# Kernel optimization log

Hardware: AMD Instinct MI355X
Metric: run time of the kernel (lower is better)

## Reference

```python
import jax, jax.numpy as jnp
import numpy as np

# Fixed architecture constants from Cifar10Model / RetNetConfig
NL = 8            # num_layers
H = 4             # num_heads
D = 64            # hidden_size
QK = 64           # qk_dim
V = 128           # v_dim
QH, VH = QK // H, V // H   # 16, 32 per-head dims
P, IMG, C = 8, 32, 3       # patch size, image size, channels
NP = (IMG // P) ** 2       # 16 patches
T = NP + 1                 # +1 cls token -> 17 tokens
FFN = 12                   # ffn_proj_size


def layer_norm(x, s, b, eps=1e-5):
    mu = x.mean(-1, keepdims=True)
    var = x.var(-1, keepdims=True)
    return (x - mu) * jax.lax.rsqrt(var + eps) * s + b


def rotate_every_two(x):
    x1, x2 = x[..., ::2], x[..., 1::2]
    return jnp.stack([-x2, x1], axis=-1).reshape(x.shape)


def rel_pos(t):
    # xPos-style rotation angles over the per-head qk dim
    angle = 1.0 / (10000 ** jnp.linspace(0.0, 1.0, QH // 2))
    angle = jnp.repeat(angle, 2)                      # (QH,)
    idx = jnp.arange(t, dtype=jnp.float32)[:, None]
    sin, cos = jnp.sin(idx * angle), jnp.cos(idx * angle)   # (t, QH)
    # per-head retention decay gamma (use_default_gamma=False path)
    gamma = 1.0 - jnp.exp(jnp.linspace(np.log(1 / 32), np.log(1 / 512), H))  # (H,)
    n = jnp.arange(t)
    expo = n[:, None] - n[None, :]                    # n - m
    causal = expo >= 0
    dmask = jnp.where(causal, gamma[:, None, None] ** jnp.where(causal, expo, 0), 0.0)  # (H,t,t)
    dmask = dmask / jnp.sqrt(dmask.sum(-1, keepdims=True))   # row-normalized decay
    return sin, cos, dmask


def retention(x, Wq, Wk, Wv, Wg, Wo, sin, cos, dmask):
    b, t, _ = x.shape
    q = (x @ Wq).reshape(b, t, H, QH).transpose(0, 2, 1, 3)   # (b,h,t,qh)
    k = (x @ Wk).reshape(b, t, H, QH).transpose(0, 2, 1, 3)
    v = (x @ Wv).reshape(b, t, H, VH).transpose(0, 2, 1, 3)   # (b,h,t,vh)
    g = x @ Wg                                                # (b,t,V) gate
    q = q * cos + rotate_every_two(q) * sin
    k = (k * cos + rotate_every_two(k) * sin) * (QH ** -0.5)
    scores = jnp.einsum('bhnd,bhmd->bhnm', q, k) * dmask      # decay-masked QK^T
    denom = jnp.clip(jnp.abs(jax.lax.stop_gradient(scores).sum(-1, keepdims=True)), 1.0, None)
    scores = scores / denom                                   # retention row normalization
    o = jnp.einsum('bhnm,bhmd->bhnd', scores, v)              # (b,h,t,vh)
    # per-head group norm (no affine) instead of softmax normalization
    mu = o.mean(-1, keepdims=True)
    var = o.var(-1, keepdims=True)
    o = (o - mu) * jax.lax.rsqrt(var + 1e-5)
    o = o.transpose(0, 2, 1, 3).reshape(b, t, V)
    return (jax.nn.silu(g) * o) @ Wo


def setup_inputs() -> dict:
    key = jax.random.key(0)
    ks = iter(jax.random.split(key, 32))
    s = 0.02
    B = 8192
    inp = {
        'x': jax.random.normal(next(ks), (B, C, IMG, IMG), jnp.float32),
        'patch_w': jax.random.normal(next(ks), (C * P * P, D), jnp.float32) * s,
        'patch_b': jnp.zeros((D,), jnp.float32),
        'cls': jax.random.normal(next(ks), (1, 1, D), jnp.float32) * s,
        'pos': jax.random.normal(next(ks), (T, D), jnp.float32) * s,
        'Wq': jax.random.normal(next(ks), (NL, D, QK), jnp.float32) * s,
        'Wk': jax.random.normal(next(ks), (NL, D, QK), jnp.float32) * s,
        'Wv': jax.random.normal(next(ks), (NL, D, V), jnp.float32) * s,
        'Wg': jax.random.normal(next(ks), (NL, D, V), jnp.float32) * s,
        'Wo': jax.random.normal(next(ks), (NL, V, D), jnp.float32) * s,
        'ln1_s': jnp.ones((NL, D), jnp.float32),
        'ln1_b': jnp.zeros((NL, D), jnp.float32),
        'w1': jax.random.normal(next(ks), (NL, D, FFN), jnp.float32) * s,
        'b1': jnp.zeros((NL, FFN), jnp.float32),
        'w2': jax.random.normal(next(ks), (NL, FFN, D), jnp.float32) * s,
        'b2': jnp.zeros((NL, D), jnp.float32),
        'ln2_s': jnp.ones((NL, D), jnp.float32),
        'ln2_b': jnp.zeros((NL, D), jnp.float32),
        'lnf_s': jnp.ones((D,), jnp.float32),
        'lnf_b': jnp.zeros((D,), jnp.float32),
        'neck_w': jax.random.normal(next(ks), (D, 16), jnp.float32) * s,
        'neck_b': jnp.zeros((16,), jnp.float32),
        'head_w': jax.random.normal(next(ks), (16, 10), jnp.float32) * s,
        'head_b': jnp.zeros((10,), jnp.float32),
    }
    return inp


def reference(x, patch_w, patch_b, cls, pos, Wq, Wk, Wv, Wg, Wo, ln1_s, ln1_b,
              w1, b1, w2, b2, ln2_s, ln2_b, lnf_s, lnf_b, neck_w, neck_b, head_w, head_b):
    b = x.shape[0]
    # patch embedding: stride==kernel conv expressed as reshape + matmul
    xp = x.reshape(b, C, IMG // P, P, IMG // P, P).transpose(0, 2, 4, 1, 3, 5)
    xp = xp.reshape(b, NP, C * P * P)
    tok = xp @ patch_w + patch_b                          # (b,16,64)
    tok = jnp.concatenate([jnp.broadcast_to(cls, (b, 1, D)), tok], axis=1) + pos  # (b,17,64)
    sin, cos, dmask = rel_pos(T)
    h = tok
    for i in range(NL):  # pre-LN RetNet blocks
        h = h + retention(layer_norm(h, ln1_s[i], ln1_b[i]),
                          Wq[i], Wk[i], Wv[i], Wg[i], Wo[i], sin, cos, dmask)
        f = layer_norm(h, ln2_s[i], ln2_b[i])
        h = h + jax.nn.gelu(f @ w1[i] + b1[i]) @ w2[i] + b2[i]
    h = layer_norm(h, lnf_s, lnf_b)
    ys = h[:, -1, :]                                      # last token
    return (ys @ neck_w + neck_b) @ head_w + head_b       # (b,10) logits
```

## Files before the change

kernel.cpp:

```cpp
#include <hip/hip_runtime.h>
#include <hip/hip_bf16.h>

#define NLAY 8
#define MFMA __builtin_amdgcn_mfma_f32_16x16x32_bf16
#define MFMA32 __builtin_amdgcn_mfma_f32_32x32x16_bf16

typedef __attribute__((ext_vector_type(8))) short bf16x8;
typedef __attribute__((ext_vector_type(4))) float f32x4;
typedef __attribute__((ext_vector_type(16))) float f32x16;
typedef __attribute__((ext_vector_type(4))) int i32x4;

template <bool BF16>
__device__ __forceinline__ float ld(const void* p, int i) {
  if (BF16) {
    unsigned short u = ((const unsigned short*)p)[i];
    return __uint_as_float(((unsigned)u) << 16);
  }
  return ((const float*)p)[i];
}

template <bool BF16>
__device__ __forceinline__ float2 ld2(const void* p, int i) {
  float2 r;
  if (BF16) {
    unsigned u = ((const unsigned*)p)[i >> 1];
    r.x = __uint_as_float(u << 16);
    r.y = __uint_as_float(u & 0xffff0000u);
  } else {
    r = ((const float2*)p)[i >> 1];
  }
  return r;
}

__device__ __forceinline__ float bfu(unsigned short u) {
  return __uint_as_float(((unsigned)u) << 16);
}

__device__ __forceinline__ unsigned pack_bf2(float a, float b) {
  __hip_bfloat16 ha = __float2bfloat16(a), hb = __float2bfloat16(b);
  unsigned short ua, ub;
  __builtin_memcpy(&ua, &ha, 2);
  __builtin_memcpy(&ub, &hb, 2);
  return ((unsigned)ub << 16) | (unsigned)ua;
}

__device__ __forceinline__ unsigned short cvt_bf(float a) {
  __hip_bfloat16 h = __float2bfloat16(a);
  unsigned short us;
  __builtin_memcpy(&us, &h, 2);
  return us;
}

__device__ __forceinline__ float2 unpk(unsigned u) {
  float2 r;
  r.x = __uint_as_float(u << 16);
  r.y = __uint_as_float(u & 0xffff0000u);
  return r;
}

__device__ __forceinline__ bf16x8 as_bf(i32x4 v) {
  bf16x8 r;
  __builtin_memcpy(&r, &v, 16);
  return r;
}

__global__ void setup_tables(float* __restrict__ ws, const void* __restrict__ x) {
  int tid = threadIdx.x;
  for (int idx = tid; idx < 272; idx += 256) {
    int t = idx >> 4, j = idx & 15;
    float a = powf(10000.f, -(float)(j >> 1) / 7.f);
    float arg = (float)t * a;
    ws[idx] = sinf(arg);
    ws[272 + idx] = cosf(arg);
  }
  for (int row = tid; row < 68; row += 256) {
    int hh = row / 17, t = row % 17;
    float gamma = 1.f - exp2f(-5.f - 4.f * (float)hh / 3.f);
    float sum = 0.f;
    for (int u = 0; u <= t; ++u) sum += powf(gamma, (float)(t - u));
    float rn = rsqrtf(sum);
    for (int u = 0; u < 17; ++u)
      ws[544 + row * 17 + u] = (u <= t) ? powf(gamma, (float)(t - u)) * rn : 0.f;
  }
  if (tid == 0) {
    const unsigned short* u16 = (const unsigned short*)x;
    int sane = 0;
    for (int i = 0; i < 128; ++i) {
      float v = __uint_as_float(((unsigned)u16[2 * i]) << 16);
      float av = fabsf(v);
      if (v == 0.f || (av > 1e-8f && av < 1e4f)) sane++;
    }
    ws[1700] = (sane >= 64) ? 1.f : 0.f;
  }
}

#define FRAG_OLD 280576
#define FRAG_TOT 305152
template <bool BF16>
__global__ void prep_frags(const void* __restrict__ patch_w,
                           const void* __restrict__ Wq, const void* __restrict__ Wk,
                           const void* __restrict__ Wv, const void* __restrict__ Wg,
                           const void* __restrict__ Wo, const void* __restrict__ w1,
                           const void* __restrict__ w2,
                           const float* __restrict__ tab,
                           unsigned short* __restrict__ frag) {
  if ((tab[1700] > 0.5f) != BF16) return;
  int g = blockIdx.x * 256 + threadIdx.x;
  if (g >= FRAG_TOT) return;
  float v;
  if (g < 12288) {
    int nt = g / 3072, r = g % 3072, kt = r / 512, r2 = r % 512, la = r2 >> 3, j = r2 & 7;
    int n = nt * 16 + (la & 15), k = kt * 32 + (la >> 4) * 8 + j;
    v = ld<BF16>(patch_w, k * 64 + n);
  } else if (g < FRAG_OLD) {
    int gg = g - 12288, l = gg / 33536, o = gg % 33536;
    if (o < 8192) {
      const void* W = (o < 4096) ? Wq : Wk;
      int e = o & 4095;
      int nt = e / 1024, r = e % 1024, kt = r / 512, r2 = r % 512, la = r2 >> 3, j = r2 & 7;
      int n = nt * 16 + (la & 15), k = kt * 32 + (la >> 4) * 8 + j;
      v = ld<BF16>(W, l * 4096 + k * 64 + n);
    } else if (o < 24576) {
      const void* W = (o < 16384) ? Wv : Wg;
      int e = (o - 8192) & 8191;
      int nt = e / 1024, r = e % 1024, kt = r / 512, r2 = r % 512, la = r2 >> 3, j = r2 & 7;
      int n = nt * 16 + (la & 15), k = kt * 32 + (la >> 4) * 8 + j;
      v = ld<BF16>(W, l * 8192 + k * 128 + n);
    } else if (o < 32768) {
      int e = o - 24576;
      int nt = e / 2048, r = e % 2048, kt = r / 512, r2 = r % 512, la = r2 >> 3, j = r2 & 7;
      int n = nt * 16 + (la & 15), k = kt * 32 + (la >> 4) * 8 + j;
      v = ld<BF16>(Wo, l * 8192 + k * 64 + n);
    } else {
      int e = o - 32768, eo = e / 64, d = e % 64;
      v = ld<BF16>(w1, l * 768 + d * 12 + eo);
    }
  } else {
    int gg = g - FRAG_OLD, l = gg / 3072, o = gg % 3072;
    if (o < 1024) {
      int kt = o >> 9, r = o & 511, la = r >> 3, j = r & 7;
      int n = la & 15, k = kt * 32 + (la >> 4) * 8 + j;
      v = (n < 12) ? ld<BF16>(w1, l * 768 + k * 12 + n) : 0.f;
    } else {
      int e2 = o - 1024;
      int nt = e2 >> 9, r = e2 & 511, la = r >> 3, j = r & 7;
      int n = nt * 16 + (la & 15), k = (la >> 4) * 8 + j;
      v = (k < 12) ? ld<BF16>(w2, (l * 12 + k) * 64 + n) : 0.f;
    }
  }
  __hip_bfloat16 h = __float2bfloat16(v);
  unsigned short us;
  __builtin_memcpy(&us, &h, 2);
  frag[g] = us;
}

#define O_DM   0
#define O_SIN  1156
#define O_COS  1428
#define O_ST   1700
#define O_H    2212
#define O_XNF  4456
#define O_FF   5992
#define O_R    6400
#define O_SCA  11024
#define O_VG   14096
#define SM_TOT 18968

template <bool BF16>
__global__ void __launch_bounds__(512, 4)
vit_fused(const void* __restrict__ x, const void* __restrict__ patch_b,
          const void* __restrict__ cls, const void* __restrict__ pos,
          const void* __restrict__ ln1s, const void* __restrict__ ln1b,
          const void* __restrict__ b1, const void* __restrict__ b2,
          const void* __restrict__ ln2s, const void* __restrict__ ln2b,
          const void* __restrict__ lnfs, const void* __restrict__ lnfb,
          const void* __restrict__ neckw, const void* __restrict__ neckb,
          const void* __restrict__ headw, const void* __restrict__ headb,
          const float* __restrict__ tab, const unsigned short* __restrict__ FR,
          void* __restrict__ out) {
  if ((tab[1700] > 0.5f) != BF16) return;

  const int tid = threadIdx.x;
  const int lane = tid & 63, w = tid >> 6;
  const int lq = lane >> 4, ln = lane & 15;
  const int img0 = 2 * blockIdx.x;

  __shared__ __align__(16) float sm[SM_TOT];
  float* sDM  = sm + O_DM;
  float* sSin = sm + O_SIN;
  float* sCos = sm + O_COS;
  float* sST  = sm + O_ST;
  float* sH   = sm + O_H;
  float* sFF  = sm + O_FF;
  float* sQ   = sm + O_R;
  float* sK   = sm + O_R + 2312;
  float* sO   = sm + O_R;
  float* sSC  = sm + O_SCA;
  unsigned short* sVbT = (unsigned short*)(sm + O_VG);
  unsigned short* sGb  = (unsigned short*)(sm + O_VG) + 5120;
  const bf16x8* FRB = (const bf16x8*)FR;

  for (int i = tid; i < 1156; i += 512) sDM[i] = tab[544 + i] * 0.25f;
  for (int i = tid; i < 272; i += 512) { sSin[i] = tab[i]; sCos[i] = tab[272 + i]; }
  for (int s = tid; s < 768; s += 512) {
    int mt = s / 384, r = s % 384, kt = r / 64, la = r % 64;
    int p = la & 15, q = la >> 4;
    int kb = kt * 32 + q * 8;
    int c = kb >> 6, rem = kb & 63, a = rem >> 3;
    int pi = p >> 2, pj = p & 3;
    int src = (img0 + mt) * 3072 + c * 1024 + (pi * 8 + a) * 32 + pj * 8;
    float v[8];
#pragma unroll
    for (int t2 = 0; t2 < 8; t2 += 2) {
      float2 pv = ld2<BF16>(x, src + t2);
      v[t2] = pv.x; v[t2 + 1] = pv.y;
    }
    i32x4 pk;
    pk.x = pack_bf2(v[0], v[1]); pk.y = pack_bf2(v[2], v[3]);
    pk.z = pack_bf2(v[4], v[5]); pk.w = pack_bf2(v[6], v[7]);
    ((i32x4*)(sm + O_SCA))[s] = pk;
  }
  if (tid < 128) {
    int img = tid >> 6, n = tid & 63;
    sH[(img * 17) * 66 + n] = ld<BF16>(cls, n) + ld<BF16>(pos, n);
  }
  __syncthreads();

  {
    int mt = w >> 2, nt = w & 3;
    f32x4 acc = {0.f, 0.f, 0.f, 0.f};
    const bf16x8* paf = (const bf16x8*)(sm + O_SCA);
#pragma unroll
    for (int kt = 0; kt < 6; ++kt)
      acc = MFMA(paf[(mt * 6 + kt) * 64 + lane], FRB[(nt * 6 + kt) * 64 + lane], acc, 0, 0, 0);
    int n = nt * 16 + ln;
    float pb = ld<BF16>(patch_b, n);
#pragma unroll
    for (int i = 0; i < 4; ++i) {
      int t = 1 + lq * 4 + i;
      sH[(mt * 17 + t) * 66 + n] = acc[i] + pb + ld<BF16>(pos, t * 64 + n);
    }
  }
  __syncthreads();

  for (int l = 0; l < NLAY; ++l) {
    const int LB = 1536 + l * 4192;

    if (tid < 272) {
      int m = tid >> 3, sub = tid & 7;
      const float2* hp = (const float2*)(sH + m * 66 + sub * 8);
      float s1 = 0.f, s2 = 0.f;
#pragma unroll
      for (int i = 0; i < 4; ++i) {
        float2 v = hp[i];
        s1 += v.x; s2 += v.x * v.x;
        s1 += v.y; s2 += v.y * v.y;
      }
      s1 += __shfl_xor(s1, 1); s2 += __shfl_xor(s2, 1);
      s1 += __shfl_xor(s1, 2); s2 += __shfl_xor(s2, 2);
      s1 += __shfl_xor(s1, 4); s2 += __shfl_xor(s2, 4);
      if (sub == 0) {
        float mu = s1 * (1.f / 64.f);
        float var = s2 * (1.f / 64.f) - mu * mu;
        sST[m] = mu;
        sST[34 + m] = rsqrtf(var + 1e-5f);
      }
    }
    __syncthreads();

    if (tid < 384) {
      int s = tid;
      int mt = s >> 7, kt = (s >> 6) & 1, la = s & 63;
      int m = mt * 16 + (la & 15), q = la >> 4;
      int kb = kt * 32 + q * 8;
      i32x4 pk = {0, 0, 0, 0};
      if (m < 34) {
        float mu = sST[m], rr = sST[34 + m];
        float vv[8];
#pragma unroll
        for (int t2 = 0; t2 < 8; t2 += 2) {
          float2 sv = ld2<BF16>(ln1s, l * 64 + kb + t2);
          float2 bv = ld2<BF16>(ln1b, l * 64 + kb + t2);
          vv[t2]     = (sH[m * 66 + kb + t2] - mu) * rr * sv.x + bv.x;
          vv[t2 + 1] = (sH[m * 66 + kb + t2 + 1] - mu) * rr * sv.y + bv.y;
        }
        pk.x = pack_bf2(vv[0], vv[1]); pk.y = pack_bf2(vv[2], vv[3]);
        pk.z = pack_bf2(vv[4], vv[5]); pk.w = pack_bf2(vv[6], vv[7]);
      }
      ((i32x4*)(sm + O_XNF))[s] = pk;
    }
    __syncthreads();

    {
      const bf16x8* xnf = (const bf16x8*)(sm + O_XNF);
      {
        const bf16x8* wf = FRB + LB + ((w < 4) ? 0 : 512);
        float* dst = (w < 4) ? sQ : sK;
        int ntl = w & 3;
        int n = ntl * 16 + ln;
#pragma unroll
        for (int mt = 0; mt < 3; ++mt) {
          f32x4 acc = {0.f, 0.f, 0.f, 0.f};
          acc = MFMA(xnf[(mt * 2) * 64 + lane], wf[(ntl * 2) * 64 + lane], acc, 0, 0, 0);
          acc = MFMA(xnf[(mt * 2 + 1) * 64 + lane], wf[(ntl * 2 + 1) * 64 + lane], acc, 0, 0, 0);
          if (mt < 2) {
            float* p = dst + (mt * 16 + lq * 4) * 68 + n;
            p[0] = acc[0]; p[68] = acc[1]; p[136] = acc[2]; p[204] = acc[3];
          } else if (lq == 0) {
            float* p = dst + 32 * 68 + n;
            p[0] = acc[0]; p[68] = acc[1];
          }
        }
      }
      {
        const bf16x8* wf = FRB + LB + 1024;
        int n = w * 16 + ln;
#pragma unroll
        for (int mt = 0; mt < 3; ++mt) {
          f32x4 acc = {0.f, 0.f, 0.f, 0.f};
          acc = MFMA(xnf[(mt * 2) * 64 + lane], wf[(w * 2) * 64 + lane], acc, 0, 0, 0);
          acc = MFMA(xnf[(mt * 2 + 1) * 64 + lane], wf[(w * 2 + 1) * 64 + lane], acc, 0, 0, 0);
          if (mt == 0) {
            uint2 uv;
            uv.x = pack_bf2(acc[0], acc[1]);
            uv.y = pack_bf2(acc[2], acc[3]);
            *(uint2*)(sVbT + n * 20 + lq * 4) = uv;
          } else if (mt == 1) {
#pragma unroll
            for (int i = 0; i < 4; ++i) {
              int m = 16 + lq * 4 + i;
              int img = (m >= 17), t = m - img * 17;
              sVbT[img * 2560 + n * 20 + t] = cvt_bf(acc[i]);
            }
          } else if (lq == 0) {
            sVbT[2560 + n * 20 + 15] = cvt_bf(acc[0]);
            sVbT[2560 + n * 20 + 16] = cvt_bf(acc[1]);
          }
        }
      }
      {
        const bf16x8* wf = FRB + LB + 2048;
        int n = w * 16 + ln;
#pragma unroll
        for (int mt = 0; mt < 3; ++mt) {
          f32x4 acc = {0.f, 0.f, 0.f, 0.f};
          acc = MFMA(xnf[(mt * 2) * 64 + lane], wf[(w * 2) * 64 + lane], acc, 0, 0, 0);
          acc = MFMA(xnf[(mt * 2 + 1) * 64 + lane], wf[(w * 2 + 1) * 64 + lane], acc, 0, 0, 0);
          if (mt < 2) {
            unsigned short* p = sGb + (mt * 16 + lq * 4) * 136 + n;
            p[0] = cvt_bf(acc[0]); p[136] = cvt_bf(acc[1]);
            p[272] = cvt_bf(acc[2]); p[408] = cvt_bf(acc[3]);
          } else if (lq == 0) {
            sGb[32 * 136 + n] = cvt_bf(acc[0]);
            sGb[33 * 136 + n] = cvt_bf(acc[1]);
          }
        }
      }
    }
    __syncthreads();

    {
      int img = w >> 2, hh = w & 3;
      int cl = lane & 31, kh = lane >> 5;
      int tt = (cl < 17) ? cl : 16;
      int rb = (img * 17 + tt) * 68 + hh * 16 + kh * 8;
      int sb = tt * 16 + kh * 8;
      float4 s0 = *(const float4*)(sSin + sb), s1 = *(const float4*)(sSin + sb + 4);
      float4 c0 = *(const float4*)(sCos + sb), c1 = *(const float4*)(sCos + sb + 4);
      float4 qa = *(const float4*)(sQ + rb), qb = *(const float4*)(sQ + rb + 4);
      i32x4 ap;
      ap.x = pack_bf2(qa.x * c0.x - qa.y * s0.x, qa.y * c0.y + qa.x * s0.y);
      ap.y = pack_bf2(qa.z * c0.z - qa.w * s0.z, qa.w * c0.w + qa.z * s0.w);
      ap.z = pack_bf2(qb.x * c1.x - qb.y * s1.x, qb.y * c1.y + qb.x * s1.y);
      ap.w = pack_bf2(qb.z * c1.z - qb.w * s1.z, qb.w * c1.w + qb.z * s1.w);
      float4 ka = *(const float4*)(sK + rb), kb = *(const float4*)(sK + rb + 4);
      i32x4 bp;
      bp.x = pack_bf2(ka.x * c0.x - ka.y * s0.x, ka.y * c0.y + ka.x * s0.y);
      bp.y = pack_bf2(ka.z * c0.z - ka.w * s0.z, ka.w * c0.w + ka.z * s0.w);
      bp.z = pack_bf2(kb.x * c1.x - kb.y * s1.x, kb.y * c1.y + kb.x * s1.y);
      bp.w = pack_bf2(kb.z * c1.z - kb.w * s1.z, kb.w * c1.w + kb.z * s1.w);
      f32x16 acc = {0.f, 0.f, 0.f, 0.f, 0.f, 0.f, 0.f, 0.f,
                    0.f, 0.f, 0.f, 0.f, 0.f, 0.f, 0.f, 0.f};
      acc = MFMA32(as_bf(ap), as_bf(bp), acc, 0, 0, 0);
      if (cl < 17) {
        int scb = img * 1360 + hh * 340;
        const float* dmb = sDM + hh * 289;
#pragma unroll
        for (int r = 0; r < 16; ++r) {
          int t = (r & 3) + 8 * (r >> 2) + 4 * kh;
          if (t < 17) sSC[scb + t * 20 + cl] = acc[r] * dmb[t * 17 + cl];
        }
      }
    }
    __syncthreads();

    if (tid < 136) {
      const float* base = sSC + tid * 20;
      float s = 0.f;
      for (int u = 0; u < 17; ++u) s += base[u];
      float den = fabsf(s);
      if (den < 1.f) den = 1.f;
      sST[68 + tid] = 1.f / den;
    }
    __syncthreads();

    {
      int img = w >> 2, hh = w & 3;
      int cl = lane & 31, kh = lane >> 5;
      int tt = (cl < 17) ? cl : 16;
      const float* scb = sSC + img * 1360 + hh * 340;
      float den = sST[68 + img * 68 + hh * 17 + tt];
      const float4* a4 = (const float4*)(scb + tt * 20 + kh * 8);
      float4 av0 = a4[0], av1 = a4[1];
      i32x4 ap;
      ap.x = pack_bf2(av0.x * den, av0.y * den);
      ap.y = pack_bf2(av0.z * den, av0.w * den);
      ap.z = pack_bf2(av1.x * den, av1.y * den);
      ap.w = pack_bf2(av1.z * den, av1.w * den);
      const unsigned short* vcol = sVbT + img * 2560 + (hh * 32 + cl) * 20 + kh * 8;
      const uint2* vq = (const uint2*)vcol;
      uint2 v0 = vq[0], v1 = vq[1];
      i32x4 bp; bp.x = (int)v0.x; bp.y = (int)v0.y; bp.z = (int)v1.x; bp.w = (int)v1.y;
      f32x16 acc = {0.f, 0.f, 0.f, 0.f, 0.f, 0.f, 0.f, 0.f,
                    0.f, 0.f, 0.f, 0.f, 0.f, 0.f, 0.f, 0.f};
      acc = MFMA32(as_bf(ap), as_bf(bp), acc, 0, 0, 0);
      i32x4 a1 = {0, 0, 0, 0}, b1v = {0, 0, 0, 0};
      if (kh == 0) {
        float s16 = scb[tt * 20 + 16] * den;
        a1.x = (int)(unsigned)cvt_bf(s16);
        b1v.x = (int)(unsigned)sVbT[img * 2560 + (hh * 32 + cl) * 20 + 16];
      }
      acc = MFMA32(as_bf(a1), as_bf(b1v), acc, 0, 0, 0);
      int cg = hh * 32 + cl;
#pragma unroll
      for (int r = 0; r < 16; ++r) {
        int t = (r & 3) + 8 * (r >> 2) + 4 * kh;
        if (t < 17) sO[(img * 17 + t) * 130 + cg] = acc[r];
      }
    }
    __syncthreads();

    if (tid < 272) {
      int row = tid >> 1, sub = tid & 1;
      int img = row / 68, hr = row % 68, hh = hr / 17, t = hr % 17;
      int m = img * 17 + t;
      const float2* op = (const float2*)(sO + m * 130 + hh * 32 + sub * 16);
      float s1 = 0.f, s2 = 0.f;
#pragma unroll
      for (int i = 0; i < 8; ++i) {
        float2 v = op[i];
        s1 += v.x; s2 += v.x * v.x;
        s1 += v.y; s2 += v.y * v.y;
      }
      s1 += __shfl_xor(s1, 1); s2 += __shfl_xor(s2, 1);
      if (sub == 0) {
        float mu = s1 * (1.f / 32.f);
        float var = s2 * (1.f / 32.f) - mu * mu;
        sST[204 + row] = mu;
        sST[340 + row] = rsqrtf(var + 1e-5f);
      }
    }
    __syncthreads();

    for (int s = tid; s < 768; s += 512) {
      int mt = s >> 8, kt = (s >> 6) & 3, la = s & 63;
      int q = la >> 4, m = mt * 16 + (la & 15);
      int cb = kt * 32 + q * 8;
      i32x4 pk = {0, 0, 0, 0};
      if (m < 34) {
        int img = (m >= 17), t = m - img * 17;
        int sti = img * 68 + kt * 17 + t;
        float mu = sST[204 + sti], rr = sST[340 + sti];
        const float2* op = (const float2*)(sO + m * 130 + cb);
        i32x4 gu = *(const i32x4*)(sGb + m * 136 + cb);
        float vv[8];
#pragma unroll
        for (int q2 = 0; q2 < 4; ++q2) {
          float2 ov = op[q2];
          unsigned gw = (q2 == 0) ? (unsigned)gu.x : (q2 == 1) ? (unsigned)gu.y
                       : (q2 == 2) ? (unsigned)gu.z : (unsigned)gu.w;
          float2 gv = unpk(gw);
          float on0 = (ov.x - mu) * rr;
          float on1 = (ov.y - mu) * rr;
          vv[2 * q2]     = on0 * (gv.x / (1.f + __expf(-gv.x)));
          vv[2 * q2 + 1] = on1 * (gv.y / (1.f + __expf(-gv.y)));
        }
        pk.x = pack_bf2(vv[0], vv[1]); pk.y = pack_bf2(vv[2], vv[3]);
        pk.z = pack_bf2(vv[4], vv[5]); pk.w = pack_bf2(vv[6], vv[7]);
      }
      ((i32x4*)(sm + O_SCA))[s] = pk;
    }
    __syncthreads();

    {
      const bf16x8* oaf = (const bf16x8*)(sm + O_SCA);
      const bf16x8* wof = FRB + LB + 3072;
      for (int j = w; j < 12; j += 8) {
        int mt = j >> 2, nt = j & 3;
        f32x4 acc = {0.f, 0.f, 0.f, 0.f};
#pragma unroll
        for (int kt = 0; kt < 4; ++kt)
          acc = MFMA(oaf[(mt * 4 + kt) * 64 + lane], wof[(nt * 4 + kt) * 64 + lane], acc, 0, 0, 0);
        int n = nt * 16 + ln;
#pragma unroll
        for (int i = 0; i < 4; ++i) {
          int m = mt * 16 + lq * 4 + i;
          if (m < 34) sH[m * 66 + n] += acc[i];
        }
      }
    }
    __syncthreads();

    if (tid < 272) {
      int m = tid >> 3, sub = tid & 7;
      const float2* hp = (const float2*)(sH + m * 66 + sub * 8);
      float s1 = 0.f, s2 = 0.f;
#pragma unroll
      for (int i = 0; i < 4; ++i) {
        float2 v = hp[i];
        s1 += v.x; s2 += v.x * v.x;
        s1 += v.y; s2 += v.y * v.y;
      }
      s1 += __shfl_xor(s1, 1); s2 += __shfl_xor(s2, 1);
      s1 += __shfl_xor(s1, 2); s2 += __shfl_xor(s2, 2);
      s1 += __shfl_xor(s1, 4); s2 += __shfl_xor(s2, 4);
      if (sub == 0) {
        float mu = s1 * (1.f / 64.f);
        float var = s2 * (1.f / 64.f) - mu * mu;
        sST[m] = mu;
        sST[34 + m] = rsqrtf(var + 1e-5f);
      }
    }
    __syncthreads();

    if (tid < 384) {
      int s = tid;
      int mt = s >> 7, kt = (s >> 6) & 1, la = s & 63;
      int m = mt * 16 + (la & 15), q = la >> 4;
      int kb = kt * 32 + q * 8;
      i32x4 pk = {0, 0, 0, 0};
      if (m < 34) {
        float mu = sST[m], rr = sST[34 + m];
        float vv[8];
#pragma unroll
        for (int t2 = 0; t2 < 8; t2 += 2) {
          float2 sv = ld2<BF16>(ln2s, l * 64 + kb + t2);
          float2 bv = ld2<BF16>(ln2b, l * 64 + kb + t2);
          vv[t2]     = (sH[m * 66 + kb + t2] - mu) * rr * sv.x + bv.x;
          vv[t2 + 1] = (sH[m * 66 + kb + t2 + 1] - mu) * rr * sv.y + bv.y;
        }
        pk.x = pack_bf2(vv[0], vv[1]); pk.y = pack_bf2(vv[2], vv[3]);
        pk.z = pack_bf2(vv[4], vv[5]); pk.w = pack_bf2(vv[6], vv[7]);
      }
      ((i32x4*)(sm + O_XNF))[s] = pk;
    }
    __syncthreads();

    if (w < 3) {
      const bf16x8* xnf = (const bf16x8*)(sm + O_XNF);
      const bf16x8* w1f = FRB + 35072 + l * 384;
      int mt = w;
      f32x4 acc = {0.f, 0.f, 0.f, 0.f};
#pragma unroll
      for (int kt = 0; kt < 2; ++kt)
        acc = MFMA(xnf[(mt * 2 + kt) * 64 + lane], w1f[kt * 64 + lane], acc, 0, 0, 0);
      if (ln < 12) {
        float b = ld<BF16>(b1, l * 12 + ln);
#pragma unroll
        for (int i = 0; i < 4; ++i) {
          int m = mt * 16 + lq * 4 + i;
          if (m < 34) {
            float a = acc[i] + b;
            float inner = 0.7978845608028654f * (a + 0.044715f * a * a * a);
            float e = __expf(2.f * inner);
            float th = 1.f - 2.f / (e + 1.f);
            sFF[m * 12 + ln] = 0.5f * a * (1.f + th);
          }
        }
      }
    }
    __syncthreads();

    {
      const bf16x8* w2f = FRB + 35072 + l * 384 + 128;
      for (int j = w; j < 12; j += 8) {
        int mt = j >> 2, nt = j & 3;
        i32x4 ap = {0, 0, 0, 0};
        int ma = mt * 16 + ln;
        if (ma < 34) {
          const float* fp = sFF + ma * 12;
          if (lq == 0) {
            ap.x = pack_bf2(fp[0], fp[1]); ap.y = pack_bf2(fp[2], fp[3]);
            ap.z = pack_bf2(fp[4], fp[5]); ap.w = pack_bf2(fp[6], fp[7]);
          } else if (lq == 1) {
            ap.x = pack_bf2(fp[8], fp[9]); ap.y = pack_bf2(fp[10], fp[11]);
          }
        }
        f32x4 acc = {0.f, 0.f, 0.f, 0.f};
        acc = MFMA(as_bf(ap), w2f[nt * 64 + lane], acc, 0, 0, 0);
        int n = nt * 16 + ln;
        float b = ld<BF16>(b2, l * 64 + n);
#pragma unroll
        for (int i = 0; i < 4; ++i) {
          int m = mt * 16 + lq * 4 + i;
          if (m < 34) sH[m * 66 + n] += acc[i] + b;
        }
      }
    }
    __syncthreads();
  }

  if (tid < 2) {
    int m = tid * 17 + 16;
    float s1 = 0.f, s2 = 0.f;
    for (int d = 0; d < 64; ++d) {
      float v = sH[m * 66 + d];
      s1 += v; s2 += v * v;
    }
    float mu = s1 * (1.f / 64.f);
    float var = s2 * (1.f / 64.f) - mu * mu;
    sST[tid] = mu;
    sST[2 + tid] = rsqrtf(var + 1e-5f);
  }
  __syncthreads();
  if (tid < 32) {
    int img = tid >> 4, jn = tid & 15;
    int m = img * 17 + 16;
    float mu = sST[img], rr = sST[2 + img];
    float acc = ld<BF16>(neckb, jn);
    for (int d = 0; d < 64; ++d) {
      float yn = (sH[m * 66 + d] - mu) * rr * ld<BF16>(lnfs, d) + ld<BF16>(lnfb, d);
      acc += yn * ld<BF16>(neckw, d * 16 + jn);
    }
    sST[8 + img * 16 + jn] = acc;
  }
  __syncthreads();
  if (tid < 20) {
    int img = tid / 10, o = tid % 10;
    float acc = ld<BF16>(headb, o);
#pragma unroll
    for (int e = 0; e < 16; ++e) acc += sST[8 + img * 16 + e] * ld<BF16>(headw, e * 10 + o);
    if (BF16) {
      ((__hip_bfloat16*)out)[(img0 + img) * 10 + o] = __float2bfloat16(acc);
    } else {
      ((float*)out)[(img0 + img) * 10 + o] = acc;
    }
  }
}

extern "C" void kernel_launch(void* const* d_in, const int* in_sizes, int n_in,
                              void* d_out, int out_size, void* d_ws, size_t ws_size,
                              hipStream_t stream) {
  float* tab = (float*)d_ws;
  unsigned short* frag = (unsigned short*)((char*)d_ws + 8192);

  setup_tables<<<dim3(1), dim3(256), 0, stream>>>(tab, d_in[0]);

  const int prepBlocks = (FRAG_TOT + 255) / 256;
  prep_frags<false><<<dim3(prepBlocks), dim3(256), 0, stream>>>(
      d_in[1], d_in[5], d_in[6], d_in[7], d_in[8], d_in[9], d_in[12], d_in[14], tab, frag);
  prep_frags<true><<<dim3(prepBlocks), dim3(256), 0, stream>>>(
      d_in[1], d_in[5], d_in[6], d_in[7], d_in[8], d_in[9], d_in[12], d_in[14], tab, frag);

  const int B = in_sizes[0] / 3072;
  const int grid = B / 2;

  vit_fused<false><<<dim3(grid), dim3(512), 0, stream>>>(
      d_in[0], d_in[2], d_in[3], d_in[4], d_in[10], d_in[11], d_in[13],
      d_in[15], d_in[16], d_in[17], d_in[18], d_in[19], d_in[20], d_in[21],
      d_in[22], d_in[23], tab, frag, d_out);
  vit_fused<true><<<dim3(grid), dim3(512), 0, stream>>>(
      d_in[0], d_in[2], d_in[3], d_in[4], d_in[10], d_in[11], d_in[13],
      d_in[15], d_in[16], d_in[17], d_in[18], d_in[19], d_in[20], d_in[21],
      d_in[22], d_in[23], tab, frag, d_out);
}
```

Baseline: 827.6 us.

## Fuse layernorm stats into normalization passes and drop intermediate barriers

Layernorm statistics for LN1, LN2 and the per-head group norm are now computed by the same threads that apply the normalization and pack bf16 fragments. Reductions use wave shuffles, so the separate stats pass, its shared-memory round trip and one barrier each go away. The retention row-denominator pass is likewise folded into the score-times-V stage, where each lane sums its whole row. This removes several __syncthreads per layer in exchange for some redundant loads and arithmetic, plus a remapped fragment slot layout that must match the MFMA operand order.

```diff
diff --git a/kernel.cpp b/kernel.cpp
--- a/kernel.cpp
+++ b/kernel.cpp
@@ -30,10 +30,6 @@
     r = ((const float2*)p)[i >> 1];
   }
   return r;
-}
-
-__device__ __forceinline__ float bfu(unsigned short u) {
-  return __uint_as_float(((unsigned)u) << 16);
 }
 
 __device__ __forceinline__ unsigned pack_bf2(float a, float b) {
@@ -246,48 +242,38 @@
   for (int l = 0; l < NLAY; ++l) {
     const int LB = 1536 + l * 4192;
 
-    if (tid < 272) {
+    if (tid < 320) {
       int m = tid >> 3, sub = tid & 7;
-      const float2* hp = (const float2*)(sH + m * 66 + sub * 8);
-      float s1 = 0.f, s2 = 0.f;
-#pragma unroll
-      for (int i = 0; i < 4; ++i) {
-        float2 v = hp[i];
-        s1 += v.x; s2 += v.x * v.x;
-        s1 += v.y; s2 += v.y * v.y;
-      }
-      s1 += __shfl_xor(s1, 1); s2 += __shfl_xor(s2, 1);
-      s1 += __shfl_xor(s1, 2); s2 += __shfl_xor(s2, 2);
-      s1 += __shfl_xor(s1, 4); s2 += __shfl_xor(s2, 4);
-      if (sub == 0) {
+      i32x4 pk = {0, 0, 0, 0};
+      if (m < 34) {
+        const float2* hp = (const float2*)(sH + m * 66 + sub * 8);
+        float2 h0 = hp[0], h1 = hp[1], h2 = hp[2], h3 = hp[3];
+        float s1 = 0.f, s2 = 0.f;
+        s1 += h0.x; s2 += h0.x * h0.x; s1 += h0.y; s2 += h0.y * h0.y;
+        s1 += h1.x; s2 += h1.x * h1.x; s1 += h1.y; s2 += h1.y * h1.y;
+        s1 += h2.x; s2 += h2.x * h2.x; s1 += h2.y; s2 += h2.y * h2.y;
+        s1 += h3.x; s2 += h3.x * h3.x; s1 += h3.y; s2 += h3.y * h3.y;
+        s1 += __shfl_xor(s1, 1); s2 += __shfl_xor(s2, 1);
+        s1 += __shfl_xor(s1, 2); s2 += __shfl_xor(s2, 2);
+        s1 += __shfl_xor(s1, 4); s2 += __shfl_xor(s2, 4);
         float mu = s1 * (1.f / 64.f);
         float var = s2 * (1.f / 64.f) - mu * mu;
-        sST[m] = mu;
-        sST[34 + m] = rsqrtf(var + 1e-5f);
-      }
-    }
-    __syncthreads();
-
-    if (tid < 384) {
-      int s = tid;
-      int mt = s >> 7, kt = (s >> 6) & 1, la = s & 63;
-      int m = mt * 16 + (la & 15), q = la >> 4;
-      int kb = kt * 32 + q * 8;
-      i32x4 pk = {0, 0, 0, 0};
-      if (m < 34) {
-        float mu = sST[m], rr = sST[34 + m];
+        float rr = rsqrtf(var + 1e-5f);
+        int kb = sub * 8;
+        float hv[8] = {h0.x, h0.y, h1.x, h1.y, h2.x, h2.y, h3.x, h3.y};
         float vv[8];
 #pragma unroll
         for (int t2 = 0; t2 < 8; t2 += 2) {
           float2 sv = ld2<BF16>(ln1s, l * 64 + kb + t2);
           float2 bv = ld2<BF16>(ln1b, l * 64 + kb + t2);
-          vv[t2]     = (sH[m * 66 + kb + t2] - mu) * rr * sv.x + bv.x;
-          vv[t2 + 1] = (sH[m * 66 + kb + t2 + 1] - mu) * rr * sv.y + bv.y;
+          vv[t2]     = (hv[t2] - mu) * rr * sv.x + bv.x;
+          vv[t2 + 1] = (hv[t2 + 1] - mu) * rr * sv.y + bv.y;
         }
         pk.x = pack_bf2(vv[0], vv[1]); pk.y = pack_bf2(vv[2], vv[3]);
         pk.z = pack_bf2(vv[4], vv[5]); pk.w = pack_bf2(vv[6], vv[7]);
       }
-      ((i32x4*)(sm + O_XNF))[s] = pk;
+      int slot = (m >> 4) * 128 + (sub >> 2) * 64 + (sub & 3) * 16 + (m & 15);
+      ((i32x4*)(sm + O_XNF))[slot] = pk;
     }
     __syncthreads();
 
@@ -394,24 +380,28 @@
     }
     __syncthreads();
 
-    if (tid < 136) {
-      const float* base = sSC + tid * 20;
-      float s = 0.f;
-      for (int u = 0; u < 17; ++u) s += base[u];
-      float den = fabsf(s);
-      if (den < 1.f) den = 1.f;
-      sST[68 + tid] = 1.f / den;
-    }
-    __syncthreads();
-
     {
       int img = w >> 2, hh = w & 3;
       int cl = lane & 31, kh = lane >> 5;
       int tt = (cl < 17) ? cl : 16;
       const float* scb = sSC + img * 1360 + hh * 340;
-      float den = sST[68 + img * 68 + hh * 17 + tt];
-      const float4* a4 = (const float4*)(scb + tt * 20 + kh * 8);
-      float4 av0 = a4[0], av1 = a4[1];
+      const float* rowp = scb + tt * 20;
+      float4 p0 = *(const float4*)(rowp);
+      float4 p1 = *(const float4*)(rowp + 4);
+      float4 p2 = *(const float4*)(rowp + 8);
+      float4 p3 = *(const float4*)(rowp + 12);
+      float s16v = rowp[16];
+      float s = 0.f;
+      s += p0.x; s += p0.y; s += p0.z; s += p0.w;
+      s += p1.x; s += p1.y; s += p1.z; s += p1.w;
+      s += p2.x; s += p2.y; s += p2.z; s += p2.w;
+      s += p3.x; s += p3.y; s += p3.z; s += p3.w;
+      s += s16v;
+      float den = fabsf(s);
+      if (den < 1.f) den = 1.f;
+      den = 1.f / den;
+      float4 av0 = (kh == 0) ? p0 : p2;
+      float4 av1 = (kh == 0) ? p1 : p3;
       i32x4 ap;
       ap.x = pack_bf2(av0.x * den, av0.y * den);
       ap.y = pack_bf2(av0.z * den, av0.w * den);
@@ -426,7 +416,7 @@
       acc = MFMA32(as_bf(ap), as_bf(bp), acc, 0, 0, 0);
       i32x4 a1 = {0, 0, 0, 0}, b1v = {0, 0, 0, 0};
       if (kh == 0) {
-        float s16 = scb[tt * 20 + 16] * den;
+        float s16 = s16v * den;
         a1.x = (int)(unsigned)cvt_bf(s16);
         b1v.x = (int)(unsigned)sVbT[img * 2560 + (hh * 32 + cl) * 20 + 16];
       }
@@ -436,28 +426,6 @@
       for (int r = 0; r < 16; ++r) {
         int t = (r & 3) + 8 * (r >> 2) + 4 * kh;
         if (t < 17) sO[(img * 17 + t) * 130 + cg] = acc[r];
-      }
-    }
-    __syncthreads();
-
-    if (tid < 272) {
-      int row = tid >> 1, sub = tid & 1;
-      int img = row / 68, hr = row % 68, hh = hr / 17, t = hr % 17;
-      int m = img * 17 + t;
-      const float2* op = (const float2*)(sO + m * 130 + hh * 32 + sub * 16);
-      float s1 = 0.f, s2 = 0.f;
-#pragma unroll
-      for (int i = 0; i < 8; ++i) {
-        float2 v = op[i];
-        s1 += v.x; s2 += v.x * v.x;
-        s1 += v.y; s2 += v.y * v.y;
-      }
-      s1 += __shfl_xor(s1, 1); s2 += __shfl_xor(s2, 1);
-      if (sub == 0) {
-        float mu = s1 * (1.f / 32.f);
-        float var = s2 * (1.f / 32.f) - mu * mu;
-        sST[204 + row] = mu;
-        sST[340 + row] = rsqrtf(var + 1e-5f);
       }
     }
     __syncthreads();
@@ -468,20 +436,28 @@
       int cb = kt * 32 + q * 8;
       i32x4 pk = {0, 0, 0, 0};
       if (m < 34) {
-        int img = (m >= 17), t = m - img * 17;
-        int sti = img * 68 + kt * 17 + t;
-        float mu = sST[204 + sti], rr = sST[340 + sti];
         const float2* op = (const float2*)(sO + m * 130 + cb);
+        float2 o0 = op[0], o1 = op[1], o2 = op[2], o3 = op[3];
+        float s1 = 0.f, s2 = 0.f;
+        s1 += o0.x; s2 += o0.x * o0.x; s1 += o0.y; s2 += o0.y * o0.y;
+        s1 += o1.x; s2 += o1.x * o1.x; s1 += o1.y; s2 += o1.y * o1.y;
+        s1 += o2.x; s2 += o2.x * o2.x; s1 += o2.y; s2 += o2.y * o2.y;
+        s1 += o3.x; s2 += o3.x * o3.x; s1 += o3.y; s2 += o3.y * o3.y;
+        s1 += __shfl_xor(s1, 16); s2 += __shfl_xor(s2, 16);
+        s1 += __shfl_xor(s1, 32); s2 += __shfl_xor(s2, 32);
+        float mu = s1 * (1.f / 32.f);
+        float var = s2 * (1.f / 32.f) - mu * mu;
+        float rr = rsqrtf(var + 1e-5f);
         i32x4 gu = *(const i32x4*)(sGb + m * 136 + cb);
+        float ov[8] = {o0.x, o0.y, o1.x, o1.y, o2.x, o2.y, o3.x, o3.y};
         float vv[8];
 #pragma unroll
         for (int q2 = 0; q2 < 4; ++q2) {
-          float2 ov = op[q2];
           unsigned gw = (q2 == 0) ? (unsigned)gu.x : (q2 == 1) ? (unsigned)gu.y
                        : (q2 == 2) ? (unsigned)gu.z : (unsigned)gu.w;
           float2 gv = unpk(gw);
-          float on0 = (ov.x - mu) * rr;
-          float on1 = (ov.y - mu) * rr;
+          float on0 = (ov[2 * q2] - mu) * rr;
+          float on1 = (ov[2 * q2 + 1] - mu) * rr;
           vv[2 * q2]     = on0 * (gv.x / (1.f + __expf(-gv.x)));
           vv[2 * q2 + 1] = on1 * (gv.y / (1.f + __expf(-gv.y)));
         }
@@ -511,48 +487,38 @@
     }
     __syncthreads();
 
-    if (tid < 272) {
+    if (tid < 320) {
       int m = tid >> 3, sub = tid & 7;
-      const float2* hp = (const float2*)(sH + m * 66 + sub * 8);
-      float s1 = 0.f, s2 = 0.f;
-#pragma unroll
-      for (int i = 0; i < 4; ++i) {
-        float2 v = hp[i];
-        s1 += v.x; s2 += v.x * v.x;
-        s1 += v.y; s2 += v.y * v.y;
-      }
-      s1 += __shfl_xor(s1, 1); s2 += __shfl_xor(s2, 1);
-      s1 += __shfl_xor(s1, 2); s2 += __shfl_xor(s2, 2);
-      s1 += __shfl_xor(s1, 4); s2 += __shfl_xor(s2, 4);
-      if (sub == 0) {
+      i32x4 pk = {0, 0, 0, 0};
+      if (m < 34) {
+        const float2* hp = (const float2*)(sH + m * 66 + sub * 8);
+        float2 h0 = hp[0], h1 = hp[1], h2 = hp[2], h3 = hp[3];
+        float s1 = 0.f, s2 = 0.f;
+        s1 += h0.x; s2 += h0.x * h0.x; s1 += h0.y; s2 += h0.y * h0.y;
+        s1 += h1.x; s2 += h1.x * h1.x; s1 += h1.y; s2 += h1.y * h1.y;
+        s1 += h2.x; s2 += h2.x * h2.x; s1 += h2.y; s2 += h2.y * h2.y;
+        s1 += h3.x; s2 += h3.x * h3.x; s1 += h3.y; s2 += h3.y * h3.y;
+        s1 += __shfl_xor(s1, 1); s2 += __shfl_xor(s2, 1);
+        s1 += __shfl_xor(s1, 2); s2 += __shfl_xor(s2, 2);
+        s1 += __shfl_xor(s1, 4); s2 += __shfl_xor(s2, 4);
         float mu = s1 * (1.f / 64.f);
         float var = s2 * (1.f / 64.f) - mu * mu;
-        sST[m] = mu;
-        sST[34 + m] = rsqrtf(var + 1e-5f);
-      }
-    }
-    __syncthreads();
-
-    if (tid < 384) {
-      int s = tid;
-      int mt = s >> 7, kt = (s >> 6) & 1, la = s & 63;
-      int m = mt * 16 + (la & 15), q = la >> 4;
-      int kb = kt * 32 + q * 8;
-      i32x4 pk = {0, 0, 0, 0};
-      if (m < 34) {
-        float mu = sST[m], rr = sST[34 + m];
+        float rr = rsqrtf(var + 1e-5f);
+        int kb = sub * 8;
+        float hv[8] = {h0.x, h0.y, h1.x, h1.y, h2.x, h2.y, h3.x, h3.y};
         float vv[8];
 #pragma unroll
         for (int t2 = 0; t2 < 8; t2 += 2) {
           float2 sv = ld2<BF16>(ln2s, l * 64 + kb + t2);
           float2 bv = ld2<BF16>(ln2b, l * 64 + kb + t2);
-          vv[t2]     = (sH[m * 66 + kb + t2] - mu) * rr * sv.x + bv.x;
-          vv[t2 + 1] = (sH[m * 66 + kb + t2 + 1] - mu) * rr * sv.y + bv.y;
+          vv[t2]     = (hv[t2] - mu) * rr * sv.x + bv.x;
+          vv[t2 + 1] = (hv[t2 + 1] - mu) * rr * sv.y + bv.y;
         }
         pk.x = pack_bf2(vv[0], vv[1]); pk.y = pack_bf2(vv[2], vv[3]);
         pk.z = pack_bf2(vv[4], vv[5]); pk.w = pack_bf2(vv[6], vv[7]);
       }
-      ((i32x4*)(sm + O_XNF))[s] = pk;
+      int slot = (m >> 4) * 128 + (sub >> 2) * 64 + (sub & 3) * 16 + (m & 15);
+      ((i32x4*)(sm + O_XNF))[slot] = pk;
     }
     __syncthreads();
 
```

After: 791.1 us. 1.05x faster.
